# Kernel tuning notes

Hardware: AMD Instinct MI355X
Metric: run time of the kernel (lower is better)

## Reference

```python
import jax, jax.numpy as jnp
import numpy as np

B_SZ = 64            # oft_block_size
IN_F = 4096
OUT_F = 4096
R_IN = IN_F // B_SZ   # 64 blocks
R_OUT = OUT_F // B_SZ # 64 blocks
N_TRI = B_SZ * (B_SZ - 1) // 2  # 2016 packed strict-upper entries
NUM_NEUMANN = 5

_rows, _cols = np.triu_indices(B_SZ, k=1)
ROWS = jnp.asarray(_rows, dtype=jnp.int32)
COLS = jnp.asarray(_cols, dtype=jnp.int32)


def setup_inputs() -> dict:
    key = jax.random.key(0)
    k = jax.random.split(key, 5)
    x = jax.random.normal(k[0], (4, 2048, IN_F), dtype=jnp.float32)
    # small skew entries so the Neumann series approximates the Cayley transform
    Ro = jax.random.normal(k[1], (R_OUT, N_TRI), dtype=jnp.float32) * 0.01
    Ri = jax.random.normal(k[2], (R_IN, N_TRI), dtype=jnp.float32) * 0.01
    W = jax.random.normal(k[3], (OUT_F, IN_F), dtype=jnp.float32) * (1.0 / np.sqrt(IN_F))
    bias = jax.random.normal(k[4], (OUT_F,), dtype=jnp.float32) * 0.01
    rng = np.random.default_rng(0)
    perm_in = rng.permutation(IN_F)
    perm_in_inv = np.argsort(perm_in)
    perm_out = rng.permutation(OUT_F)
    return {
        "x": x, "Ro": Ro, "Ri": Ri, "W": W, "bias": bias,
        "perm_in_inv": jnp.asarray(perm_in_inv, dtype=jnp.int32),
        "perm_out": jnp.asarray(perm_out, dtype=jnp.int32),
    }


def _skew(vec):
    # vec: (r, n_tri) packed strict-upper entries -> (r, b, b) skew-symmetric
    r = vec.shape[0]
    M = jnp.zeros((r, B_SZ, B_SZ), dtype=vec.dtype).at[:, ROWS, COLS].set(vec)
    return M - jnp.swapaxes(M, -2, -1)


def _cayley_neumann(Q):
    # R = I + 2*(Q + Q^2 + Q^3 + Q^4)   (num_neumann_terms = 5)
    I = jnp.eye(B_SZ, dtype=Q.dtype)
    acc = Q
    Qp = Q
    for _ in range(3, NUM_NEUMANN):
        pass
    Q2 = jnp.matmul(Q, Q)
    acc = acc + Q2
    Qp = Q2
    for _ in range(3, NUM_NEUMANN):
        Qp = jnp.matmul(Qp, Q)
        acc = acc + Qp
    return I + 2.0 * acc


def reference(x, Ro, Ri, W, bias, perm_in_inv, perm_out):
    R_out = _cayley_neumann(_skew(Ro))   # (r_out, b, b)
    R_in = _cayley_neumann(_skew(Ri))    # (r_in, b, b)

    B, S, _ = x.shape
    xp = x[..., perm_in_inv]                               # input permutation
    xb = xp.reshape(B, S, R_IN, B_SZ)
    xR = jnp.einsum('bsrc,rcd->bsrd', xb, R_in)            # block-diag right rotate
    y = xR.reshape(B, S, IN_F) @ W.T + bias                # base linear
    yb = y.reshape(B, S, R_OUT, B_SZ)
    yR = jnp.einsum('bsrc,rcd->bsrd', yb, R_out)           # block-diag output rotate
    out = yR.reshape(B, S, OUT_F)[..., perm_out]           # output permutation
    return out
```

## Files before the change

kernel.cpp:

```cpp
#include <hip/hip_runtime.h>
#include <stdint.h>

#define IN_F 4096
#define OUT_F 4096
#define NTRI 2016

typedef unsigned short u16;
typedef __attribute__((ext_vector_type(8))) short short8;
typedef __attribute__((ext_vector_type(4))) float f32x4;
typedef __attribute__((ext_vector_type(4))) int i32x4;
typedef __attribute__((ext_vector_type(4))) unsigned short u16x4;

__device__ __forceinline__ u16 f2bf(float f) {
    uint32_t u = __builtin_bit_cast(uint32_t, f);
    u = (u + 0x7FFFu + ((u >> 16) & 1u)) >> 16;
    return (u16)u;
}

__device__ __forceinline__ void gload16(const void* g, void* l) {
    __builtin_amdgcn_global_load_lds((__attribute__((address_space(1))) void*)g,
                                     (__attribute__((address_space(3))) void*)l,
                                     16, 0, 0);
}

__global__ __launch_bounds__(256) void k_prep(const float* __restrict__ Ro,
                                              const float* __restrict__ Ri,
                                              const int* __restrict__ perm_out,
                                              const float* __restrict__ x,
                                              const int* __restrict__ pii,
                                              float* __restrict__ Rout,
                                              u16* __restrict__ QT16,
                                              u16* __restrict__ P16,
                                              int* __restrict__ pinv_out,
                                              u16* __restrict__ xb) {
    const int b = blockIdx.x;
    const int t = threadIdx.x;
    if (b == 128) {
#pragma unroll
        for (int e = 0; e < 16; ++e) {
            int i = e * 256 + t;
            pinv_out[perm_out[i]] = i;
        }
        return;
    }
    if (b >= 129) {
        __shared__ __align__(16) float xr[4096];
        const int blk = b - 129;
        int pv[16];
#pragma unroll
        for (int q = 0; q < 4; ++q) *(i32x4*)&pv[q * 4] = *(const i32x4*)&pii[t * 16 + q * 4];
        for (int r = 0; r < 8; ++r) {
            size_t srow = (size_t)blk * 8 + r;
            const float* src = x + srow * 4096;
#pragma unroll
            for (int q = 0; q < 4; ++q)
                *(f32x4*)&xr[q * 1024 + t * 4] = *(const f32x4*)&src[q * 1024 + t * 4];
            __syncthreads();
            union { short8 v; u16 e[8]; } o0, o1;
#pragma unroll
            for (int j = 0; j < 8; ++j) { o0.e[j] = f2bf(xr[pv[j]]); o1.e[j] = f2bf(xr[pv[8 + j]]); }
            *(short8*)&xb[srow * 4096 + t * 16] = o0.v;
            *(short8*)&xb[srow * 4096 + t * 16 + 8] = o1.v;
            __syncthreads();
        }
        return;
    }
    __shared__ __align__(16) float Qs[64 * 64];
    __shared__ __align__(16) float Ps[64 * 68];
    __shared__ __align__(16) float Ts[64 * 68];
    const float* vec = (b < 64) ? (Ro + (size_t)b * NTRI) : (Ri + (size_t)(b - 64) * NTRI);
    int tr = t >> 4, tc = t & 15;
#pragma unroll
    for (int e = 0; e < 16; ++e) {
        int el = e * 256 + t;
        int i = el >> 6, j = el & 63;
        float q = 0.f;
        if (i < j) q =  vec[i * 63 - (i * (i - 1)) / 2 + (j - i - 1)];
        if (i > j) q = -vec[j * 63 - (j * (j - 1)) / 2 + (i - j - 1)];
        Qs[el] = q;
    }
    __syncthreads();
    float a2[4][4], a3[4][4], a4[4][4];
#pragma unroll
    for (int i = 0; i < 4; ++i)
#pragma unroll
        for (int j = 0; j < 4; ++j) { a2[i][j] = 0.f; a3[i][j] = 0.f; a4[i][j] = 0.f; }
    for (int k = 0; k < 64; ++k) {
        f32x4 qa = *(const f32x4*)&Qs[k * 64 + tr * 4];
        f32x4 qb = *(const f32x4*)&Qs[k * 64 + tc * 4];
#pragma unroll
        for (int i = 0; i < 4; ++i)
#pragma unroll
            for (int j = 0; j < 4; ++j) a2[i][j] -= qa[i] * qb[j];
    }
#pragma unroll
    for (int i = 0; i < 4; ++i)
#pragma unroll
        for (int j = 0; j < 4; ++j) Ps[(tr * 4 + i) * 68 + tc * 4 + j] = a2[i][j];
    __syncthreads();
    for (int k = 0; k < 64; ++k) {
        f32x4 pa = *(const f32x4*)&Ps[k * 68 + tr * 4];
        f32x4 qb = *(const f32x4*)&Qs[k * 64 + tc * 4];
#pragma unroll
        for (int i = 0; i < 4; ++i)
#pragma unroll
            for (int j = 0; j < 4; ++j) a3[i][j] += pa[i] * qb[j];
    }
#pragma unroll
    for (int i = 0; i < 4; ++i)
#pragma unroll
        for (int j = 0; j < 4; ++j) Ts[(tc * 4 + j) * 68 + tr * 4 + i] = -a3[i][j];
    __syncthreads();
    for (int k = 0; k < 64; ++k) {
        f32x4 ta = *(const f32x4*)&Ts[k * 68 + tr * 4];
        f32x4 qb = *(const f32x4*)&Qs[k * 64 + tc * 4];
#pragma unroll
        for (int i = 0; i < 4; ++i)
#pragma unroll
            for (int j = 0; j < 4; ++j) a4[i][j] -= ta[i] * qb[j];
    }
    if (b < 64) {
        float* dst = Rout + (size_t)b * 4096;
        u16* qt = QT16 + (size_t)b * 4096;
#pragma unroll
        for (int i = 0; i < 4; ++i) {
            int gi = tr * 4 + i;
            f32x4 q4 = *(const f32x4*)&Qs[gi * 64 + tc * 4];
            f32x4 o;
#pragma unroll
            for (int j = 0; j < 4; ++j) {
                int gj = tc * 4 + j;
                o[j] = 2.f * (q4[j] + a2[i][j] + a3[i][j] + a4[i][j]) + ((gi == gj) ? 1.f : 0.f);
            }
            *(f32x4*)&dst[gi * 64 + tc * 4] = o;
#pragma unroll
            for (int j = 0; j < 4; ++j) qt[(tc * 4 + j) * 64 + gi] = f2bf(o[j]);
        }
    } else {
        u16* p = P16 + (size_t)(b - 64) * 4096;
#pragma unroll
        for (int i = 0; i < 4; ++i) {
            int gi = tr * 4 + i;
            f32x4 q4 = *(const f32x4*)&Qs[gi * 64 + tc * 4];
            u16x4 pk;
#pragma unroll
            for (int j = 0; j < 4; ++j) {
                int gj = tc * 4 + j;
                float v = 2.f * (q4[j] + a2[i][j] + a3[i][j] + a4[i][j]) + ((gi == gj) ? 1.f : 0.f);
                pk[j] = f2bf(v);
            }
            *(u16x4*)&p[gi * 64 + tc * 4] = pk;
        }
    }
}

__global__ __launch_bounds__(256) void k_work(const float* __restrict__ W,
                                              const u16* __restrict__ P16,
                                              const u16* __restrict__ QT16,
                                              const int* __restrict__ pinv_out,
                                              const float* __restrict__ bias,
                                              const float* __restrict__ Rout,
                                              const int* __restrict__ perm_out,
                                              u16* __restrict__ Ctp,
                                              float* __restrict__ bfinal) {
    const int fb = blockIdx.x;
    const int t = threadIdx.x;
    if (fb < 2048) {
        __shared__ __align__(16) u16 Wst[128 * 64];
        __shared__ __align__(16) u16 Ut[64 * 128];
        const int s = fb & 63;
        const int br = fb >> 6;
        const int lane = t & 63;
        const int w = t >> 6;
        const int fl = lane & 15;
        const int kg = lane >> 4;

        short8 bfP[4][2];
        const u16* Pbase = P16 + (size_t)s * 4096;
#pragma unroll
        for (int nf = 0; nf < 4; ++nf)
#pragma unroll
            for (int kk = 0; kk < 2; ++kk)
                bfP[nf][kk] = *(const short8*)(Pbase + (nf * 16 + fl) * 64 + kk * 32 + kg * 8);

#pragma unroll
        for (int q = 0; q < 4; ++q) {
            int ci = q * 256 + t;
            int row = ci >> 3, slot = ci & 7;
            const float* src = W + (size_t)(br * 128 + row) * IN_F + s * 64 + slot * 8;
            f32x4 v0 = *(const f32x4*)src;
            f32x4 v1 = *(const f32x4*)(src + 4);
            union { short8 v; u16 e[8]; } cv;
            cv.e[0] = f2bf(v0[0]); cv.e[1] = f2bf(v0[1]); cv.e[2] = f2bf(v0[2]); cv.e[3] = f2bf(v0[3]);
            cv.e[4] = f2bf(v1[0]); cv.e[5] = f2bf(v1[1]); cv.e[6] = f2bf(v1[2]); cv.e[7] = f2bf(v1[3]);
            *(short8*)&Wst[row * 64 + (slot ^ (row & 7)) * 8] = cv.v;
        }
        __syncthreads();

        f32x4 acc1[2][4];
#pragma unroll
        for (int mf = 0; mf < 2; ++mf)
#pragma unroll
            for (int nf = 0; nf < 4; ++nf) acc1[mf][nf] = f32x4{0.f, 0.f, 0.f, 0.f};
#pragma unroll
        for (int mf = 0; mf < 2; ++mf) {
            int row = w * 32 + mf * 16 + fl;
#pragma unroll
            for (int kk = 0; kk < 2; ++kk) {
                short8 a = *(const short8*)&Wst[row * 64 + ((kk * 4 + kg) ^ (row & 7)) * 8];
#pragma unroll
                for (int nf = 0; nf < 4; ++nf)
                    acc1[mf][nf] = __builtin_amdgcn_mfma_f32_16x16x32_bf16(a, bfP[nf][kk], acc1[mf][nf], 0, 0, 0);
            }
        }
#pragma unroll
        for (int mf = 0; mf < 2; ++mf)
#pragma unroll
            for (int nf = 0; nf < 4; ++nf) {
                int i = nf * 16 + fl;
                int c = w * 32 + mf * 16 + kg * 4;
                u16x4 pk;
#pragma unroll
                for (int reg = 0; reg < 4; ++reg) pk[reg] = f2bf(acc1[mf][nf][reg]);
                int slot = c >> 3, half = (c >> 2) & 1;
                *(u16x4*)&Ut[i * 128 + ((slot ^ (i & 7)) << 3) + (half << 2)] = pk;
            }
        __syncthreads();

        const int rbl = w >> 1;
        const int r_g = br * 2 + rbl;
        short8 aQ[2][2];
#pragma unroll
        for (int mf2 = 0; mf2 < 2; ++mf2) {
            int d = (w & 1) * 32 + mf2 * 16 + fl;
#pragma unroll
            for (int kk = 0; kk < 2; ++kk)
                aQ[mf2][kk] = *(const short8*)(QT16 + (size_t)r_g * 4096 + d * 64 + kk * 32 + kg * 8);
        }
        f32x4 acc2[2][4];
#pragma unroll
        for (int mf2 = 0; mf2 < 2; ++mf2)
#pragma unroll
            for (int nf = 0; nf < 4; ++nf) acc2[mf2][nf] = f32x4{0.f, 0.f, 0.f, 0.f};
#pragma unroll
        for (int kk = 0; kk < 2; ++kk)
#pragma unroll
            for (int nf = 0; nf < 4; ++nf) {
                int i = nf * 16 + fl;
                int slot = rbl * 8 + kk * 4 + kg;
                short8 bu = *(const short8*)&Ut[i * 128 + ((slot ^ (i & 7)) << 3)];
#pragma unroll
                for (int mf2 = 0; mf2 < 2; ++mf2)
                    acc2[mf2][nf] = __builtin_amdgcn_mfma_f32_16x16x32_bf16(aQ[mf2][kk], bu, acc2[mf2][nf], 0, 0, 0);
            }
#pragma unroll
        for (int mf2 = 0; mf2 < 2; ++mf2)
#pragma unroll
            for (int reg = 0; reg < 4; ++reg) {
                int o_g = br * 128 + w * 32 + mf2 * 16 + kg * 4 + reg;
                int j = pinv_out[o_g];
                u16* dst = Ctp + (size_t)j * IN_F + s * 64;
#pragma unroll
                for (int nf = 0; nf < 4; ++nf)
                    dst[nf * 16 + fl] = f2bf(acc2[mf2][nf][reg]);
            }
    } else {
        int j = (fb - 2048) * 256 + t;
        int o = perm_out[j];
        int r = o >> 6, d = o & 63;
        const float* Rb = Rout + (size_t)r * 4096;
        const float* bb = bias + r * 64;
        float s = 0.f;
        for (int c = 0; c < 64; ++c) s += bb[c] * Rb[c * 64 + d];
        bfinal[j] = s;
    }
}

__global__ __launch_bounds__(512, 2) void k_gemm(const u16* __restrict__ A,
                                                 const u16* __restrict__ Bt,
                                                 const float* __restrict__ bias,
                                                 float* __restrict__ out) {
    __shared__ __align__(16) u16 lds[65536];
    const int t = threadIdx.x;
    const int lane = t & 63;
    const int wid = t >> 6;
    const int wr = wid >> 2, wc = wid & 3;

    int flat = blockIdx.y * gridDim.x + blockIdx.x;
    int swz  = (flat & 7) * 64 + (flat >> 3);
    int bm = swz >> 4;
    int bn = swz & 15;

    const int srow = t >> 2;
    const int sks  = (t & 3) ^ ((t >> 3) & 3);
    const u16* sA0 = A  + (size_t)(bm * 256 + srow) * IN_F + sks * 8;
    const u16* sA1 = sA0 + (size_t)128 * IN_F;
    const u16* sB0 = Bt + (size_t)(bn * 256 + srow) * IN_F + sks * 8;
    const u16* sB1 = sB0 + (size_t)128 * IN_F;
    u16* dA = lds + t * 8;
    u16* dB = lds + 8192 + t * 8;

    const int frow = lane & 15;
    const int kg = lane >> 4;
    const int swzr = kg ^ ((frow >> 1) & 3);
    const int aoff = (wr * 128 + frow) * 32 + swzr * 8;
    const int boff = 8192 + (wc * 64 + frow) * 32 + swzr * 8;

    f32x4 acc[8][4];
#pragma unroll
    for (int m = 0; m < 8; ++m)
#pragma unroll
        for (int n = 0; n < 4; ++n) acc[m][n] = f32x4{0.f, 0.f, 0.f, 0.f};

#pragma unroll
    for (int p = 0; p < 3; ++p) {
        int off = p * 32;
        int bb = p * 16384;
        gload16(sA0 + off, dA + bb); gload16(sA1 + off, dA + bb + 4096);
        gload16(sB0 + off, dB + bb); gload16(sB1 + off, dB + bb + 4096);
    }
    asm volatile("s_waitcnt vmcnt(8)" ::: "memory");
    __builtin_amdgcn_s_barrier();

    for (int t4 = 0; t4 < 128; t4 += 4) {
#pragma unroll
        for (int u = 0; u < 4; ++u) {
            const int kt = t4 + u;
            const u16* base = lds + u * 16384;
            short8 af[8], bf[4];
            const u16* pa = base + aoff;
            const u16* pb = base + boff;
#pragma unroll
            for (int m = 0; m < 8; ++m) af[m] = *(const short8*)(pa + m * 512);
#pragma unroll
            for (int n = 0; n < 4; ++n) bf[n] = *(const short8*)(pb + n * 512);
            {
                int ts = kt + 3;
                int tsc = ts < 128 ? ts : 124;
                int off = tsc * 32;
                int bb = ((kt + 3) & 3) * 16384;
                gload16(sA0 + off, dA + bb); gload16(sA1 + off, dA + bb + 4096);
                gload16(sB0 + off, dB + bb); gload16(sB1 + off, dB + bb + 4096);
            }
            __builtin_amdgcn_s_setprio(1);
#pragma unroll
            for (int m = 0; m < 8; ++m)
#pragma unroll
                for (int n = 0; n < 4; ++n)
                    acc[m][n] = __builtin_amdgcn_mfma_f32_16x16x32_bf16(af[m], bf[n], acc[m][n], 0, 0, 0);
            __builtin_amdgcn_s_setprio(0);
            asm volatile("s_waitcnt vmcnt(8)" ::: "memory");
            __builtin_amdgcn_s_barrier();
        }
    }
    asm volatile("s_waitcnt vmcnt(0)" ::: "memory");

    const int col0 = bn * 256 + wc * 64 + frow;
    const int row0 = bm * 256 + wr * 128 + kg * 4;
    float bv[4];
#pragma unroll
    for (int n = 0; n < 4; ++n) bv[n] = bias[col0 + n * 16];
#pragma unroll
    for (int m = 0; m < 8; ++m)
#pragma unroll
        for (int n = 0; n < 4; ++n)
#pragma unroll
            for (int i = 0; i < 4; ++i)
                out[(size_t)(row0 + m * 16 + i) * OUT_F + col0 + n * 16] = acc[m][n][i] + bv[n];
}

extern "C" void kernel_launch(void* const* d_in, const int* in_sizes, int n_in,
                              void* d_out, int out_size, void* d_ws, size_t ws_size,
                              hipStream_t stream) {
    (void)in_sizes; (void)n_in; (void)out_size; (void)ws_size;
    const float* x    = (const float*)d_in[0];
    const float* Ro   = (const float*)d_in[1];
    const float* Ri   = (const float*)d_in[2];
    const float* W    = (const float*)d_in[3];
    const float* bias = (const float*)d_in[4];
    const int* perm_in_inv = (const int*)d_in[5];
    const int* perm_out    = (const int*)d_in[6];
    float* out = (float*)d_out;

    char* ws = (char*)d_ws;
    float* Rout   = (float*)(ws);
    u16*   P16    = (u16*)(ws + (1ull << 20));
    u16*   QT16   = (u16*)(ws + (1ull << 20) + (1 << 19));
    int*   pinvo  = (int*)(ws + (2ull << 20));
    float* bfinal = (float*)(ws + (2ull << 20) + (1 << 16));
    u16*   Ctp    = (u16*)(ws + (4ull << 20));
    u16*   xb     = (u16*)(ws + (36ull << 20));

    k_prep<<<1153, 256, 0, stream>>>(Ro, Ri, perm_out, x, perm_in_inv,
                                     Rout, QT16, P16, pinvo, xb);
    k_work<<<2064, 256, 0, stream>>>(W, P16, QT16, pinvo, bias, Rout,
                                     perm_out, Ctp, bfinal);
    k_gemm<<<dim3(16, 32), 512, 0, stream>>>(xb, Ctp, bfinal, out);
}
```

Before: 318.7 us.

## Double-buffer LDS fragment loads in registers across GEMM k-steps

Restructures the bf16 MFMA main loop so that the A/B fragments for the next k-tile are read from LDS into a second register set while the MFMAs for the current tile run. The loop is unrolled by two, alternating between the two register sets, and the wait before each barrier now requires only the tile two steps ahead to have landed. The aim is to hide LDS read latency behind matrix-core work. In exchange it needs about 48 more VGPRs for the second fragment set, which could lower occupancy or cause spills, and it shortens the global-load lookahead that must be in flight at each barrier.

```diff
diff --git a/kernel.cpp b/kernel.cpp
--- a/kernel.cpp
+++ b/kernel.cpp
@@ -306,50 +306,50 @@
     const int aoff = (wr * 128 + frow) * 32 + swzr * 8;
     const int boff = 8192 + (wc * 64 + frow) * 32 + swzr * 8;
 
+#define STAGE(slot, kt) do { int bb_ = (slot) * 16384, off_ = (kt) * 32; \
+        gload16(sA0 + off_, dA + bb_); gload16(sA1 + off_, dA + bb_ + 4096); \
+        gload16(sB0 + off_, dB + bb_); gload16(sB1 + off_, dB + bb_ + 4096); } while (0)
+
+#define LOADFRAGS(AF, BF, buf) do { const u16* base_ = lds + (buf) * 16384; \
+        _Pragma("unroll") for (int m_ = 0; m_ < 8; ++m_) AF[m_] = *(const short8*)(base_ + aoff + m_ * 512); \
+        _Pragma("unroll") for (int n_ = 0; n_ < 4; ++n_) BF[n_] = *(const short8*)(base_ + boff + n_ * 512); } while (0)
+
+#define MFMAS(AF, BF) do { __builtin_amdgcn_s_setprio(1); \
+        _Pragma("unroll") for (int m_ = 0; m_ < 8; ++m_) \
+        _Pragma("unroll") for (int n_ = 0; n_ < 4; ++n_) \
+            acc[m_][n_] = __builtin_amdgcn_mfma_f32_16x16x32_bf16(AF[m_], BF[n_], acc[m_][n_], 0, 0, 0); \
+        __builtin_amdgcn_s_setprio(0); } while (0)
+
     f32x4 acc[8][4];
 #pragma unroll
     for (int m = 0; m < 8; ++m)
 #pragma unroll
         for (int n = 0; n < 4; ++n) acc[m][n] = f32x4{0.f, 0.f, 0.f, 0.f};
 
-#pragma unroll
-    for (int p = 0; p < 3; ++p) {
-        int off = p * 32;
-        int bb = p * 16384;
-        gload16(sA0 + off, dA + bb); gload16(sA1 + off, dA + bb + 4096);
-        gload16(sB0 + off, dB + bb); gload16(sB1 + off, dB + bb + 4096);
-    }
-    asm volatile("s_waitcnt vmcnt(8)" ::: "memory");
+    STAGE(0, 0); STAGE(1, 1); STAGE(2, 2);
+    asm volatile("s_waitcnt vmcnt(4)" ::: "memory");
     __builtin_amdgcn_s_barrier();
 
-    for (int t4 = 0; t4 < 128; t4 += 4) {
-#pragma unroll
-        for (int u = 0; u < 4; ++u) {
-            const int kt = t4 + u;
-            const u16* base = lds + u * 16384;
-            short8 af[8], bf[4];
-            const u16* pa = base + aoff;
-            const u16* pb = base + boff;
-#pragma unroll
-            for (int m = 0; m < 8; ++m) af[m] = *(const short8*)(pa + m * 512);
-#pragma unroll
-            for (int n = 0; n < 4; ++n) bf[n] = *(const short8*)(pb + n * 512);
-            {
-                int ts = kt + 3;
-                int tsc = ts < 128 ? ts : 124;
-                int off = tsc * 32;
-                int bb = ((kt + 3) & 3) * 16384;
-                gload16(sA0 + off, dA + bb); gload16(sA1 + off, dA + bb + 4096);
-                gload16(sB0 + off, dB + bb); gload16(sB1 + off, dB + bb + 4096);
-            }
-            __builtin_amdgcn_s_setprio(1);
-#pragma unroll
-            for (int m = 0; m < 8; ++m)
-#pragma unroll
-                for (int n = 0; n < 4; ++n)
-                    acc[m][n] = __builtin_amdgcn_mfma_f32_16x16x32_bf16(af[m], bf[n], acc[m][n], 0, 0, 0);
-            __builtin_amdgcn_s_setprio(0);
-            asm volatile("s_waitcnt vmcnt(8)" ::: "memory");
+    short8 afX[8], bfX[4], afY[8], bfY[4];
+    LOADFRAGS(afX, bfX, 0);
+
+    for (int ii = 0; ii < 64; ++ii) {
+        {
+            const int i = 2 * ii;
+            LOADFRAGS(afY, bfY, (i + 1) & 3);
+            int ts = i + 3; if (ts > 127) ts = 127;
+            STAGE((i + 3) & 3, ts);
+            MFMAS(afX, bfX);
+            asm volatile("s_waitcnt vmcnt(4)" ::: "memory");
+            __builtin_amdgcn_s_barrier();
+        }
+        {
+            const int i = 2 * ii + 1;
+            LOADFRAGS(afX, bfX, (i + 1) & 3);
+            int ts = i + 3; if (ts > 127) ts = 127;
+            STAGE((i + 3) & 3, ts);
+            MFMAS(afY, bfY);
+            asm volatile("s_waitcnt vmcnt(4)" ::: "memory");
             __builtin_amdgcn_s_barrier();
         }
     }
@@ -367,6 +367,9 @@
 #pragma unroll
             for (int i = 0; i < 4; ++i)
                 out[(size_t)(row0 + m * 16 + i) * OUT_F + col0 + n * 16] = acc[m][n][i] + bv[n];
+#undef STAGE
+#undef LOADFRAGS
+#undef MFMAS
 }
 
 extern "C" void kernel_launch(void* const* d_in, const int* in_sizes, int n_in,
```

Result: no change. 313.2 us (median of 3 runs) (-1.7%).
